# Kernel optimization log

Hardware: AMD Instinct MI355X
Metric: run time of the kernel (lower is better)

## Reference

```python
import jax, jax.numpy as jnp
import numpy as np

N_HEADS = 16
LN_EPS = 1e-5


def setup_inputs() -> dict:
    key = jax.random.key(0)
    k_z, k_qkv, k_proj = jax.random.split(key, 3)
    b, n, dm = 4, 2048, 1024
    z = jax.random.normal(k_z, (b, n, dm), dtype=jnp.float32)
    gamma = jnp.ones((dm,), dtype=jnp.float32)
    beta = jnp.zeros((dm,), dtype=jnp.float32)
    # parameterize Linear weights as (in, out) so y = x @ w (same math as torch x @ W.T)
    w_qkv = jax.random.normal(k_qkv, (dm, 3 * dm), dtype=jnp.float32) * (1.0 / np.sqrt(dm))
    w_proj = jax.random.normal(k_proj, (dm, dm), dtype=jnp.float32) * (1.0 / np.sqrt(dm))
    b_proj = jnp.zeros((dm,), dtype=jnp.float32)
    return {"z": z, "gamma": gamma, "beta": beta, "w_qkv": w_qkv,
            "w_proj": w_proj, "b_proj": b_proj}


def reference(z, gamma, beta, w_qkv, w_proj, b_proj):
    b, n, dm = z.shape
    h = N_HEADS
    d = dm // h
    scaling = jnp.asarray(np.sqrt(dm / h), dtype=z.dtype)

    # LayerNorm over last dim
    mu = jnp.mean(z, axis=-1, keepdims=True)
    var = jnp.mean(jnp.square(z - mu), axis=-1, keepdims=True)
    zn = (z - mu) * jax.lax.rsqrt(var + LN_EPS) * gamma + beta

    qkv = zn @ w_qkv  # [b, n, 3*dm]
    # einops 'b n (h d qkv_n) -> qkv_n b h n d': qkv index is INNERMOST of packed dim
    qkv = qkv.reshape(b, n, h, d, 3)
    q = qkv[..., 0]  # [b, n, h, d]
    k = qkv[..., 1]
    v = qkv[..., 2]

    scores = jnp.einsum('bqhd,bkhd->bhqk', q, k) / scaling  # [b, h, n, n]
    att = jax.nn.softmax(scores, axis=-1)
    out = jnp.einsum('bhqk,bkhd->bqhd', att, v).reshape(b, n, dm)
    out = out @ w_proj + b_proj  # projection (drop_hidden=False); dropout is identity in eval
    return z + out
```

## Files before the change

kernel.cpp:

```cpp
#include <hip/hip_runtime.h>

typedef unsigned short ushort;
typedef unsigned int uint;

typedef __bf16 bf16x8 __attribute__((ext_vector_type(8)));
typedef float floatx4 __attribute__((ext_vector_type(4)));

constexpr int BATCH = 4;
constexpr int SEQ = 2048;
constexpr int DM = 1024;
constexpr int NH = 16;
constexpr int HD = 64;
constexpr int M = BATCH * SEQ;
constexpr int NQKV = 3 * DM;
constexpr float QSCALE = 0.18033688011112042f;

__device__ __forceinline__ ushort f2b(float f) {
    uint x; __builtin_memcpy(&x, &f, 4);
    x += 0x7fffu + ((x >> 16) & 1u);
    return (ushort)(x >> 16);
}

__device__ __forceinline__ void gload16(const ushort* g, ushort* l) {
    __builtin_amdgcn_global_load_lds(
        (const __attribute__((address_space(1))) void*)g,
        (__attribute__((address_space(3))) void*)l, 16, 0, 0);
}

__global__ __launch_bounds__(256) void transpose_cast(
    const float* __restrict__ in, ushort* __restrict__ out, int R, int C) {
    __shared__ ushort tile[64][65];
    int c0 = blockIdx.x * 64, r0 = blockIdx.y * 64;
    int tx = threadIdx.x & 63, ty = threadIdx.x >> 6;
#pragma unroll
    for (int i = 0; i < 64; i += 4)
        tile[i + ty][tx] = f2b(in[(size_t)(r0 + i + ty) * C + c0 + tx]);
    __syncthreads();
#pragma unroll
    for (int i = 0; i < 64; i += 4)
        out[(size_t)(c0 + i + ty) * R + r0 + tx] = tile[tx][i + ty];
}

__global__ __launch_bounds__(256) void transpose_cast_qkv(
    const float* __restrict__ in, ushort* __restrict__ out) {
    __shared__ ushort tile[64][65];
    int c0 = blockIdx.x * 64, r0 = blockIdx.y * 64;
    int tx = threadIdx.x & 63, ty = threadIdx.x >> 6;
#pragma unroll
    for (int i = 0; i < 64; i += 4)
        tile[i + ty][tx] = f2b(in[(size_t)(r0 + i + ty) * NQKV + c0 + tx]);
    __syncthreads();
#pragma unroll
    for (int i = 0; i < 64; i += 4) {
        int c = c0 + i + ty;
        int cp = (c % 3) * DM + c / 3;
        out[(size_t)cp * DM + r0 + tx] = tile[tx][i + ty];
    }
}

__global__ __launch_bounds__(256) void ln_kernel(
    const float* __restrict__ z, const float* __restrict__ gamma,
    const float* __restrict__ beta, ushort* __restrict__ zn) {
    int row = blockIdx.x;
    int t = threadIdx.x;
    float4 v = reinterpret_cast<const float4*>(z + (size_t)row * DM)[t];
    float s = v.x + v.y + v.z + v.w;
    float sq = v.x * v.x + v.y * v.y + v.z * v.z + v.w * v.w;
#pragma unroll
    for (int off = 32; off >= 1; off >>= 1) {
        s  += __shfl_xor(s, off);
        sq += __shfl_xor(sq, off);
    }
    __shared__ float red[8];
    int wave = t >> 6;
    if ((t & 63) == 0) { red[wave] = s; red[wave + 4] = sq; }
    __syncthreads();
    s  = red[0] + red[1] + red[2] + red[3];
    sq = red[4] + red[5] + red[6] + red[7];
    float mean = s * (1.f / DM);
    float var  = sq * (1.f / DM) - mean * mean;
    float rstd = rsqrtf(var + 1e-5f);
    float4 g = reinterpret_cast<const float4*>(gamma)[t];
    float4 bt = reinterpret_cast<const float4*>(beta)[t];
    ushort4 o;
    o.x = f2b((v.x - mean) * rstd * g.x + bt.x);
    o.y = f2b((v.y - mean) * rstd * g.y + bt.y);
    o.z = f2b((v.z - mean) * rstd * g.z + bt.z);
    o.w = f2b((v.w - mean) * rstd * g.w + bt.w);
    reinterpret_cast<ushort4*>(zn + (size_t)row * DM)[t] = o;
}

__device__ __forceinline__ void gemm128_core(
    const ushort* __restrict__ A, const ushort* __restrict__ BT,
    int m0, int n0, int t, floatx4 (&acc)[4][4],
    ushort (*As)[32], ushort (*Bs)[32]) {
    int lane = t & 63, w = t >> 6;
    int l16 = lane & 15, quad = lane >> 4;
    int wm = (w >> 1) * 64, wn = (w & 1) * 64;
#pragma unroll
    for (int i = 0; i < 4; i++)
#pragma unroll
        for (int j = 0; j < 4; j++) acc[i][j] = (floatx4){0.f, 0.f, 0.f, 0.f};

    int sr = (w << 4) + (lane >> 2);
    int seg = (((lane & 3) ^ ((sr >> 1) & 3)) << 3);
    const ushort* gA0 = &A [(size_t)(m0 + sr) * DM + seg];
    const ushort* gA1 = &A [(size_t)(m0 + sr + 64) * DM + seg];
    const ushort* gB0 = &BT[(size_t)(n0 + sr) * DM + seg];
    const ushort* gB1 = &BT[(size_t)(n0 + sr + 64) * DM + seg];
    ushort* lA0 = &As[(w << 4)][0];
    ushort* lA1 = &As[64 + (w << 4)][0];
    ushort* lB0 = &Bs[(w << 4)][0];
    ushort* lB1 = &Bs[64 + (w << 4)][0];
    int sw = (l16 >> 1) & 3;

    for (int k0 = 0; k0 < DM; k0 += 32) {
        gload16(gA0 + k0, lA0);
        gload16(gA1 + k0, lA1);
        gload16(gB0 + k0, lB0);
        gload16(gB1 + k0, lB1);
        __syncthreads();
        bf16x8 af[4], bf[4];
#pragma unroll
        for (int i = 0; i < 4; i++)
            af[i] = *reinterpret_cast<const bf16x8*>(&As[wm + i * 16 + l16][(quad ^ sw) << 3]);
#pragma unroll
        for (int j = 0; j < 4; j++)
            bf[j] = *reinterpret_cast<const bf16x8*>(&Bs[wn + j * 16 + l16][(quad ^ sw) << 3]);
#pragma unroll
        for (int i = 0; i < 4; i++)
#pragma unroll
            for (int j = 0; j < 4; j++)
                acc[i][j] = __builtin_amdgcn_mfma_f32_16x16x32_bf16(af[i], bf[j], acc[i][j], 0, 0, 0);
        __syncthreads();
    }
}

__global__ __launch_bounds__(256) void gemm_qkv(
    const ushort* __restrict__ A,
    const ushort* __restrict__ BT,
    ushort* __restrict__ Q, ushort* __restrict__ K, ushort* __restrict__ V) {
    __shared__ ushort As[128][32];
    __shared__ ushort Bs[128][32];
    __shared__ ushort Cs[9216];
    int t = threadIdx.x;
    int m0 = blockIdx.y * 128, n0 = blockIdx.x * 128;
    floatx4 acc[4][4];
    gemm128_core(A, BT, m0, n0, t, acc, As, Bs);
    int lane = t & 63, w = t >> 6;
    int l16 = lane & 15, quad = lane >> 4;
    int wm = (w >> 1) * 64, wn = (w & 1) * 64;
    int which = n0 >> 10;
    int hd0 = n0 & 1023;
    float scale = (which == 0) ? QSCALE : 1.0f;
    int bb = m0 >> 11;
    int nb = m0 & 2047;
    ushort* dstQK = (which == 0) ? Q : K;

#pragma unroll
    for (int p = 0; p < 2; p++) {
        __syncthreads();
        if ((w >> 1) == p) {
            if (which < 2) {
#pragma unroll
                for (int i = 0; i < 4; i++)
#pragma unroll
                    for (int j = 0; j < 4; j++)
#pragma unroll
                        for (int r = 0; r < 4; r++)
                            Cs[(i * 16 + quad * 4 + r) * 136 + wn + j * 16 + l16] =
                                f2b(acc[i][j][r] * scale);
            } else {
#pragma unroll
                for (int i = 0; i < 4; i++)
#pragma unroll
                    for (int j = 0; j < 4; j++)
#pragma unroll
                        for (int r = 0; r < 4; r++)
                            Cs[(wn + j * 16 + l16) * 72 + i * 16 + quad * 4 + r] =
                                f2b(acc[i][j][r]);
            }
        }
        __syncthreads();
        if (which < 2) {
            int ch = (t & 15) * 8;
#pragma unroll
            for (int u = 0; u < 4; u++) {
                int lr = (t >> 4) + u * 16;
                int n = nb + p * 64 + lr;
                int hh = (hd0 + ch) >> 6, dd = ch & 63;
                *reinterpret_cast<uint4*>(
                    &dstQK[((size_t)((bb * NH + hh) * SEQ) + n) * HD + dd]) =
                    *reinterpret_cast<const uint4*>(&Cs[lr * 136 + ch]);
            }
        } else {
            int nch = (t & 7) * 8;
#pragma unroll
            for (int u = 0; u < 4; u++) {
                int dc = (t >> 3) + u * 32;
                int hh = (hd0 >> 6) + (dc >> 6), dd = dc & 63;
                int n = nb + p * 64 + nch;
                *reinterpret_cast<uint4*>(
                    &V[((size_t)((bb * NH + hh) * HD) + dd) * SEQ + n]) =
                    *reinterpret_cast<const uint4*>(&Cs[dc * 72 + nch]);
            }
        }
    }
}

__global__ __launch_bounds__(256) void gemm_proj(
    const ushort* __restrict__ A,
    const ushort* __restrict__ BT,
    const float* __restrict__ bias, const float* __restrict__ z,
    float* __restrict__ out) {
    __shared__ ushort As[128][32];
    __shared__ ushort Bs[128][32];
    int t = threadIdx.x;
    int m0 = blockIdx.y * 128, n0 = blockIdx.x * 128;
    floatx4 acc[4][4];
    gemm128_core(A, BT, m0, n0, t, acc, As, Bs);
    int lane = t & 63, w = t >> 6;
    int l16 = lane & 15, quad = lane >> 4;
    int wm = (w >> 1) * 64, wn = (w & 1) * 64;
#pragma unroll
    for (int j = 0; j < 4; j++) {
        int col = n0 + wn + j * 16 + l16;
        float bz = bias[col];
#pragma unroll
        for (int i = 0; i < 4; i++) {
#pragma unroll
            for (int r = 0; r < 4; r++) {
                int row = m0 + wm + i * 16 + quad * 4 + r;
                out[(size_t)row * DM + col] =
                    acc[i][j][r] + bz + z[(size_t)row * DM + col];
            }
        }
    }
}

__global__ __launch_bounds__(256) void attn_kernel(
    const ushort* __restrict__ Q, const ushort* __restrict__ K,
    const ushort* __restrict__ Vt, ushort* __restrict__ O) {
    __shared__ ushort QsPs[64 * 64];
    __shared__ ushort Ks[2][64 * 64];
    __shared__ ushort Vs[2][64 * 64];
    int t = threadIdx.x;
    int lane = t & 63, w = t >> 6;
    int l16 = lane & 15, quad = lane >> 4;
    int bb = blockIdx.y >> 4, h = blockIdx.y & 15;
    int q0 = blockIdx.x * 64;
    const ushort* Qg = Q  + (size_t)((bb * NH + h) * SEQ + q0) * HD;
    const ushort* Kg = K  + (size_t)((bb * NH + h) * SEQ) * HD;
    const ushort* Vg = Vt + (size_t)((bb * NH + h) * HD) * SEQ;

    int srow = lane >> 3;
    int lseg = (lane & 7) ^ srow;
    int r0 = 8 * w + srow;

    gload16(Qg + (size_t)r0 * HD + lseg * 8,        &QsPs[w * 512]);
    gload16(Qg + (size_t)(32 + r0) * HD + lseg * 8, &QsPs[2048 + w * 512]);
    gload16(Kg + (size_t)r0 * HD + lseg * 8,        &Ks[0][w * 512]);
    gload16(Kg + (size_t)(32 + r0) * HD + lseg * 8, &Ks[0][2048 + w * 512]);
    gload16(Vg + (size_t)r0 * SEQ + lseg * 8,       &Vs[0][w * 512]);
    gload16(Vg + (size_t)(32 + r0) * SEQ + lseg * 8,&Vs[0][2048 + w * 512]);
    __syncthreads();

    int swl = l16 & 7;
    bf16x8 aq0 = *reinterpret_cast<const bf16x8*>(&QsPs[(16 * w + l16) * 64 + ((quad ^ swl) << 3)]);
    bf16x8 aq1 = *reinterpret_cast<const bf16x8*>(&QsPs[(16 * w + l16) * 64 + (((quad + 4) ^ swl) << 3)]);
    ushort* PsRow = &QsPs[(16 * w + l16) * 64];

    bf16x8 bones;
    {
        union { ushort u[8]; bf16x8 v; } cvt;
        ushort one = (l16 == 0) ? (ushort)0x3F80 : (ushort)0;
#pragma unroll
        for (int i = 0; i < 8; i++) cvt.u[i] = one;
        bones = cvt.v;
    }

    floatx4 Oacc[4], lacc = (floatx4){0.f, 0.f, 0.f, 0.f};
#pragma unroll
    for (int tt = 0; tt < 4; tt++) Oacc[tt] = (floatx4){0.f, 0.f, 0.f, 0.f};

    constexpr int NT = SEQ / 64;
    for (int kt = 0; kt < NT; kt++) {
        int cur = kt & 1;
        if (kt + 1 < NT) {
            const ushort* Kn = Kg + (size_t)(kt + 1) * 64 * HD;
            const ushort* Vn = Vg + (size_t)(kt + 1) * 64;
            gload16(Kn + (size_t)r0 * HD + lseg * 8,         &Ks[cur ^ 1][w * 512]);
            gload16(Kn + (size_t)(32 + r0) * HD + lseg * 8,  &Ks[cur ^ 1][2048 + w * 512]);
            gload16(Vn + (size_t)r0 * SEQ + lseg * 8,        &Vs[cur ^ 1][w * 512]);
            gload16(Vn + (size_t)(32 + r0) * SEQ + lseg * 8, &Vs[cur ^ 1][2048 + w * 512]);
        }
        const ushort* Kc = Ks[cur];
        const ushort* Vc = Vs[cur];

        floatx4 sacc[4];
#pragma unroll
        for (int nt = 0; nt < 4; nt++) {
            bf16x8 ak0 = *reinterpret_cast<const bf16x8*>(&Kc[(nt * 16 + l16) * 64 + ((quad ^ swl) << 3)]);
            bf16x8 ak1 = *reinterpret_cast<const bf16x8*>(&Kc[(nt * 16 + l16) * 64 + (((quad + 4) ^ swl) << 3)]);
            floatx4 sv = (floatx4){0.f, 0.f, 0.f, 0.f};
            sv = __builtin_amdgcn_mfma_f32_16x16x32_bf16(ak0, aq0, sv, 0, 0, 0);
            sv = __builtin_amdgcn_mfma_f32_16x16x32_bf16(ak1, aq1, sv, 0, 0, 0);
            sacc[nt] = sv;
        }
#pragma unroll
        for (int nt = 0; nt < 4; nt++) {
            float p0 = __builtin_amdgcn_exp2f(sacc[nt][0]);
            float p1 = __builtin_amdgcn_exp2f(sacc[nt][1]);
            float p2 = __builtin_amdgcn_exp2f(sacc[nt][2]);
            float p3 = __builtin_amdgcn_exp2f(sacc[nt][3]);
            uint b0, b1, b2, b3;
            __builtin_memcpy(&b0, &p0, 4); __builtin_memcpy(&b1, &p1, 4);
            __builtin_memcpy(&b2, &p2, 4); __builtin_memcpy(&b3, &p3, 4);
            uint2 pk;
            pk.x = __builtin_amdgcn_perm(b1, b0, 0x07060302u);
            pk.y = __builtin_amdgcn_perm(b3, b2, 0x07060302u);
            int lseg2 = 2 * nt + (quad >> 1);
            *reinterpret_cast<uint2*>(&PsRow[((lseg2 ^ swl) << 3) + (quad & 1) * 4]) = pk;
        }
#pragma unroll
        for (int ks = 0; ks < 2; ks++) {
            bf16x8 ap = *reinterpret_cast<const bf16x8*>(
                &PsRow[(((4 * ks + quad) ^ swl) << 3)]);
            lacc = __builtin_amdgcn_mfma_f32_16x16x32_bf16(ap, bones, lacc, 0, 0, 0);
#pragma unroll
            for (int tt = 0; tt < 4; tt++) {
                bf16x8 bv = *reinterpret_cast<const bf16x8*>(
                    &Vc[(tt * 16 + l16) * 64 + ((((ks * 4 + quad)) ^ swl) << 3)]);
                Oacc[tt] = __builtin_amdgcn_mfma_f32_16x16x32_bf16(ap, bv, Oacc[tt], 0, 0, 0);
            }
        }
        __syncthreads();
    }
    float lq[4];
#pragma unroll
    for (int j = 0; j < 4; j++) lq[j] = __shfl(lacc[j], quad << 4);

#pragma unroll
    for (int tt = 0; tt < 4; tt++) {
#pragma unroll
        for (int j = 0; j < 4; j++) {
            int n = q0 + w * 16 + quad * 4 + j;
            int dcol = tt * 16 + l16;
            float val = Oacc[tt][j] / lq[j];
            O[(size_t)(bb * SEQ + n) * DM + h * HD + dcol] = f2b(val);
        }
    }
}

extern "C" void kernel_launch(void* const* d_in, const int* in_sizes, int n_in,
                              void* d_out, int out_size, void* d_ws, size_t ws_size,
                              hipStream_t stream) {
    const float* z      = (const float*)d_in[0];
    const float* gamma  = (const float*)d_in[1];
    const float* beta   = (const float*)d_in[2];
    const float* w_qkv  = (const float*)d_in[3];
    const float* w_proj = (const float*)d_in[4];
    const float* b_proj = (const float*)d_in[5];
    float* out = (float*)d_out;

    char* ws = (char*)d_ws;
    const size_t SZ = (size_t)M * DM * sizeof(ushort);
    ushort* zn   = (ushort*)(ws);
    ushort* Qb   = (ushort*)(ws + SZ);
    ushort* Kb   = (ushort*)(ws + 2 * SZ);
    ushort* Vb   = (ushort*)(ws + 3 * SZ);
    ushort* wqT  = (ushort*)(ws + 4 * SZ);
    ushort* wpT  = (ushort*)(ws + 4 * SZ + (size_t)DM * NQKV * sizeof(ushort));
    ushort* Ob = zn;

    dim3 tq(NQKV / 64, DM / 64);
    transpose_cast_qkv<<<tq, 256, 0, stream>>>(w_qkv, wqT);
    dim3 tp(DM / 64, DM / 64);
    transpose_cast<<<tp, 256, 0, stream>>>(w_proj, wpT, DM, DM);
    ln_kernel<<<M, 256, 0, stream>>>(z, gamma, beta, zn);
    dim3 g1(NQKV / 128, M / 128);
    gemm_qkv<<<g1, 256, 0, stream>>>(zn, wqT, Qb, Kb, Vb);
    dim3 g2(SEQ / 64, BATCH * NH);
    attn_kernel<<<g2, 256, 0, stream>>>(Qb, Kb, Vb, Ob);
    dim3 g3(DM / 128, M / 128);
    gemm_proj<<<g3, 256, 0, stream>>>(Ob, wpT, b_proj, z, out);
}
```

Measured before the change: 312.9 us.

## Process 128 query rows per attention block to reuse K/V tiles

Each attention workgroup now handles 128 queries instead of 64, with every wave owning two 16-row query groups. Each K and V fragment read from LDS is reused for two MFMA groups, halving K/V global and LDS traffic per query. The grid is also flattened to 1D, with the batch-head index varying fastest so that concurrent blocks share K/V in cache. The cost is more accumulator registers and a grid half the size (1024 blocks), which may lower occupancy. An unused variable in the QKV GEMM epilogue is also removed.

```diff
diff --git a/kernel.cpp b/kernel.cpp
--- a/kernel.cpp
+++ b/kernel.cpp
@@ -149,7 +149,7 @@
     gemm128_core(A, BT, m0, n0, t, acc, As, Bs);
     int lane = t & 63, w = t >> 6;
     int l16 = lane & 15, quad = lane >> 4;
-    int wm = (w >> 1) * 64, wn = (w & 1) * 64;
+    int wn = (w & 1) * 64;
     int which = n0 >> 10;
     int hd0 = n0 & 1023;
     float scale = (which == 0) ? QSCALE : 1.0f;
@@ -241,14 +241,16 @@
 __global__ __launch_bounds__(256) void attn_kernel(
     const ushort* __restrict__ Q, const ushort* __restrict__ K,
     const ushort* __restrict__ Vt, ushort* __restrict__ O) {
-    __shared__ ushort QsPs[64 * 64];
+    __shared__ ushort QsPs[128 * 64];
     __shared__ ushort Ks[2][64 * 64];
     __shared__ ushort Vs[2][64 * 64];
     int t = threadIdx.x;
     int lane = t & 63, w = t >> 6;
     int l16 = lane & 15, quad = lane >> 4;
-    int bb = blockIdx.y >> 4, h = blockIdx.y & 15;
-    int q0 = blockIdx.x * 64;
+    int id = blockIdx.x;
+    int qt = id >> 6, bh = id & 63;
+    int bb = bh >> 4, h = bh & 15;
+    int q0 = qt * 128;
     const ushort* Qg = Q  + (size_t)((bb * NH + h) * SEQ + q0) * HD;
     const ushort* Kg = K  + (size_t)((bb * NH + h) * SEQ) * HD;
     const ushort* Vg = Vt + (size_t)((bb * NH + h) * HD) * SEQ;
@@ -257,18 +259,26 @@
     int lseg = (lane & 7) ^ srow;
     int r0 = 8 * w + srow;
 
-    gload16(Qg + (size_t)r0 * HD + lseg * 8,        &QsPs[w * 512]);
-    gload16(Qg + (size_t)(32 + r0) * HD + lseg * 8, &QsPs[2048 + w * 512]);
-    gload16(Kg + (size_t)r0 * HD + lseg * 8,        &Ks[0][w * 512]);
-    gload16(Kg + (size_t)(32 + r0) * HD + lseg * 8, &Ks[0][2048 + w * 512]);
-    gload16(Vg + (size_t)r0 * SEQ + lseg * 8,       &Vs[0][w * 512]);
-    gload16(Vg + (size_t)(32 + r0) * SEQ + lseg * 8,&Vs[0][2048 + w * 512]);
+    gload16(Qg + (size_t)r0 * HD + lseg * 8,         &QsPs[w * 512]);
+    gload16(Qg + (size_t)(32 + r0) * HD + lseg * 8,  &QsPs[2048 + w * 512]);
+    gload16(Qg + (size_t)(64 + r0) * HD + lseg * 8,  &QsPs[4096 + w * 512]);
+    gload16(Qg + (size_t)(96 + r0) * HD + lseg * 8,  &QsPs[6144 + w * 512]);
+    gload16(Kg + (size_t)r0 * HD + lseg * 8,         &Ks[0][w * 512]);
+    gload16(Kg + (size_t)(32 + r0) * HD + lseg * 8,  &Ks[0][2048 + w * 512]);
+    gload16(Vg + (size_t)r0 * SEQ + lseg * 8,        &Vs[0][w * 512]);
+    gload16(Vg + (size_t)(32 + r0) * SEQ + lseg * 8, &Vs[0][2048 + w * 512]);
     __syncthreads();
 
     int swl = l16 & 7;
-    bf16x8 aq0 = *reinterpret_cast<const bf16x8*>(&QsPs[(16 * w + l16) * 64 + ((quad ^ swl) << 3)]);
-    bf16x8 aq1 = *reinterpret_cast<const bf16x8*>(&QsPs[(16 * w + l16) * 64 + (((quad + 4) ^ swl) << 3)]);
-    ushort* PsRow = &QsPs[(16 * w + l16) * 64];
+    bf16x8 aq[2][2];
+    ushort* PsRow[2];
+#pragma unroll
+    for (int g = 0; g < 2; g++) {
+        int row = 32 * w + 16 * g + l16;
+        aq[g][0] = *reinterpret_cast<const bf16x8*>(&QsPs[row * 64 + ((quad ^ swl) << 3)]);
+        aq[g][1] = *reinterpret_cast<const bf16x8*>(&QsPs[row * 64 + (((quad + 4) ^ swl) << 3)]);
+        PsRow[g] = &QsPs[row * 64];
+    }
 
     bf16x8 bones;
     {
@@ -279,9 +289,13 @@
         bones = cvt.v;
     }
 
-    floatx4 Oacc[4], lacc = (floatx4){0.f, 0.f, 0.f, 0.f};
-#pragma unroll
-    for (int tt = 0; tt < 4; tt++) Oacc[tt] = (floatx4){0.f, 0.f, 0.f, 0.f};
+    floatx4 Oacc[2][4], lacc[2];
+#pragma unroll
+    for (int g = 0; g < 2; g++) {
+        lacc[g] = (floatx4){0.f, 0.f, 0.f, 0.f};
+#pragma unroll
+        for (int tt = 0; tt < 4; tt++) Oacc[g][tt] = (floatx4){0.f, 0.f, 0.f, 0.f};
+    }
 
     constexpr int NT = SEQ / 64;
     for (int kt = 0; kt < NT; kt++) {
@@ -297,57 +311,74 @@
         const ushort* Kc = Ks[cur];
         const ushort* Vc = Vs[cur];
 
-        floatx4 sacc[4];
+        floatx4 sacc[2][4];
 #pragma unroll
         for (int nt = 0; nt < 4; nt++) {
             bf16x8 ak0 = *reinterpret_cast<const bf16x8*>(&Kc[(nt * 16 + l16) * 64 + ((quad ^ swl) << 3)]);
             bf16x8 ak1 = *reinterpret_cast<const bf16x8*>(&Kc[(nt * 16 + l16) * 64 + (((quad + 4) ^ swl) << 3)]);
-            floatx4 sv = (floatx4){0.f, 0.f, 0.f, 0.f};
-            sv = __builtin_amdgcn_mfma_f32_16x16x32_bf16(ak0, aq0, sv, 0, 0, 0);
-            sv = __builtin_amdgcn_mfma_f32_16x16x32_bf16(ak1, aq1, sv, 0, 0, 0);
-            sacc[nt] = sv;
-        }
-#pragma unroll
-        for (int nt = 0; nt < 4; nt++) {
-            float p0 = __builtin_amdgcn_exp2f(sacc[nt][0]);
-            float p1 = __builtin_amdgcn_exp2f(sacc[nt][1]);
-            float p2 = __builtin_amdgcn_exp2f(sacc[nt][2]);
-            float p3 = __builtin_amdgcn_exp2f(sacc[nt][3]);
-            uint b0, b1, b2, b3;
-            __builtin_memcpy(&b0, &p0, 4); __builtin_memcpy(&b1, &p1, 4);
-            __builtin_memcpy(&b2, &p2, 4); __builtin_memcpy(&b3, &p3, 4);
-            uint2 pk;
-            pk.x = __builtin_amdgcn_perm(b1, b0, 0x07060302u);
-            pk.y = __builtin_amdgcn_perm(b3, b2, 0x07060302u);
-            int lseg2 = 2 * nt + (quad >> 1);
-            *reinterpret_cast<uint2*>(&PsRow[((lseg2 ^ swl) << 3) + (quad & 1) * 4]) = pk;
+#pragma unroll
+            for (int g = 0; g < 2; g++) {
+                floatx4 sv = (floatx4){0.f, 0.f, 0.f, 0.f};
+                sv = __builtin_amdgcn_mfma_f32_16x16x32_bf16(ak0, aq[g][0], sv, 0, 0, 0);
+                sv = __builtin_amdgcn_mfma_f32_16x16x32_bf16(ak1, aq[g][1], sv, 0, 0, 0);
+                sacc[g][nt] = sv;
+            }
+        }
+#pragma unroll
+        for (int g = 0; g < 2; g++) {
+#pragma unroll
+            for (int nt = 0; nt < 4; nt++) {
+                float p0 = __builtin_amdgcn_exp2f(sacc[g][nt][0]);
+                float p1 = __builtin_amdgcn_exp2f(sacc[g][nt][1]);
+                float p2 = __builtin_amdgcn_exp2f(sacc[g][nt][2]);
+                float p3 = __builtin_amdgcn_exp2f(sacc[g][nt][3]);
+                uint b0, b1, b2, b3;
+                __builtin_memcpy(&b0, &p0, 4); __builtin_memcpy(&b1, &p1, 4);
+                __builtin_memcpy(&b2, &p2, 4); __builtin_memcpy(&b3, &p3, 4);
+                uint2 pk;
+                pk.x = __builtin_amdgcn_perm(b1, b0, 0x07060302u);
+                pk.y = __builtin_amdgcn_perm(b3, b2, 0x07060302u);
+                int lseg2 = 2 * nt + (quad >> 1);
+                *reinterpret_cast<uint2*>(&PsRow[g][((lseg2 ^ swl) << 3) + (quad & 1) * 4]) = pk;
+            }
         }
 #pragma unroll
         for (int ks = 0; ks < 2; ks++) {
-            bf16x8 ap = *reinterpret_cast<const bf16x8*>(
-                &PsRow[(((4 * ks + quad) ^ swl) << 3)]);
-            lacc = __builtin_amdgcn_mfma_f32_16x16x32_bf16(ap, bones, lacc, 0, 0, 0);
+            bf16x8 ap[2];
+#pragma unroll
+            for (int g = 0; g < 2; g++) {
+                ap[g] = *reinterpret_cast<const bf16x8*>(
+                    &PsRow[g][(((4 * ks + quad) ^ swl) << 3)]);
+                lacc[g] = __builtin_amdgcn_mfma_f32_16x16x32_bf16(ap[g], bones, lacc[g], 0, 0, 0);
+            }
 #pragma unroll
             for (int tt = 0; tt < 4; tt++) {
                 bf16x8 bv = *reinterpret_cast<const bf16x8*>(
                     &Vc[(tt * 16 + l16) * 64 + ((((ks * 4 + quad)) ^ swl) << 3)]);
-                Oacc[tt] = __builtin_amdgcn_mfma_f32_16x16x32_bf16(ap, bv, Oacc[tt], 0, 0, 0);
+#pragma unroll
+                for (int g = 0; g < 2; g++)
+                    Oacc[g][tt] = __builtin_amdgcn_mfma_f32_16x16x32_bf16(ap[g], bv, Oacc[g][tt], 0, 0, 0);
             }
         }
         __syncthreads();
     }
-    float lq[4];
-#pragma unroll
-    for (int j = 0; j < 4; j++) lq[j] = __shfl(lacc[j], quad << 4);
-
-#pragma unroll
-    for (int tt = 0; tt < 4; tt++) {
-#pragma unroll
-        for (int j = 0; j < 4; j++) {
-            int n = q0 + w * 16 + quad * 4 + j;
-            int dcol = tt * 16 + l16;
-            float val = Oacc[tt][j] / lq[j];
-            O[(size_t)(bb * SEQ + n) * DM + h * HD + dcol] = f2b(val);
+    float lq[2][4];
+#pragma unroll
+    for (int g = 0; g < 2; g++)
+#pragma unroll
+        for (int j = 0; j < 4; j++) lq[g][j] = __shfl(lacc[g][j], quad << 4);
+
+#pragma unroll
+    for (int g = 0; g < 2; g++) {
+#pragma unroll
+        for (int tt = 0; tt < 4; tt++) {
+#pragma unroll
+            for (int j = 0; j < 4; j++) {
+                int n = q0 + 32 * w + 16 * g + quad * 4 + j;
+                int dcol = tt * 16 + l16;
+                float val = Oacc[g][tt][j] / lq[g][j];
+                O[(size_t)(bb * SEQ + n) * DM + h * HD + dcol] = f2b(val);
+            }
         }
     }
 }
@@ -380,8 +411,7 @@
     ln_kernel<<<M, 256, 0, stream>>>(z, gamma, beta, zn);
     dim3 g1(NQKV / 128, M / 128);
     gemm_qkv<<<g1, 256, 0, stream>>>(zn, wqT, Qb, Kb, Vb);
-    dim3 g2(SEQ / 64, BATCH * NH);
-    attn_kernel<<<g2, 256, 0, stream>>>(Qb, Kb, Vb, Ob);
+    attn_kernel<<<(SEQ / 128) * BATCH * NH, 256, 0, stream>>>(Qb, Kb, Vb, Ob);
     dim3 g3(DM / 128, M / 128);
     gemm_proj<<<g3, 256, 0, stream>>>(Ob, wpT, b_proj, z, out);
 }
```

Result: faster. 301.1 us (-3.8%).
